# Kernel tuning notes

Hardware: AMD Instinct MI355X
Metric: run time of the kernel (lower is better)

Reference implementation:

```python
import jax, jax.numpy as jnp
import numpy as np

B, T, J, D = 32, 1024, 64, 256


def setup_inputs() -> dict:
    key = jax.random.key(0)
    k1, k2, k3, k4 = jax.random.split(key, 4)
    U = jax.random.normal(k1, (B, J, D), dtype=jnp.float32)
    H = jax.random.normal(k2, (B, T, D), dtype=jnp.float32)
    # similarity_layer: Linear(3*D, 1) -> weight [3*D], bias scalar
    w = jax.random.normal(k3, (3 * D,), dtype=jnp.float32) * (1.0 / np.sqrt(3 * D))
    b = jax.random.normal(k4, (), dtype=jnp.float32) * 0.01
    return {"U": U, "H": H, "w": w, "b": b}


def reference(U, H, w, b):
    # Linear([H; U; H*U]) decomposes exactly into three small contractions:
    # S[b,t,j] = H[b,t]@w_h + U[b,j]@w_u + (H[b,t]*w_hu)@U[b,j] + bias
    w_h, w_u, w_hu = w[:D], w[D:2 * D], w[2 * D:]
    S = (
        jnp.einsum("btd,d->bt", H, w_h)[:, :, None]
        + jnp.einsum("bjd,d->bj", U, w_u)[:, None, :]
        + jnp.einsum("btd,bjd->btj", H * w_hu, U)
        + b
    )  # [B, T, J]
    A = jax.nn.softmax(S, axis=2)                      # context-to-query attention
    c2q = jnp.einsum("btj,bjd->btd", A, U)             # [B, T, D]
    b_att = jax.nn.softmax(jnp.max(S, axis=2), axis=1)  # [B, T]
    q2c = jnp.einsum("bt,btd->bd", b_att, H)[:, None, :]  # [B, 1, D]
    G = jnp.concatenate((H, c2q, H * c2q, H * q2c), axis=2)  # [B, T, 4D]
    return (G, c2q, q2c)
```

## Files before the change

### kernel.cpp

```cpp
#include <hip/hip_runtime.h>
#include <hip/hip_bf16.h>

#define BB 32
#define TT 1024
#define JJ 64
#define DD 256

typedef __attribute__((ext_vector_type(4))) float f32x4;
__device__ __forceinline__ void nt_store4(float* addr, float4 v) {
    union { float4 a; f32x4 b; } u;
    u.a = v;
    __builtin_nontemporal_store(u.b, (f32x4*)addr);
}

__global__ __launch_bounds__(256) void k0_prep(const float* __restrict__ U,
                                               const float* __restrict__ H,
                                               const float* __restrict__ w,
                                               const float* __restrict__ bp,
                                               float* __restrict__ Up,
                                               float* __restrict__ uw,
                                               float* __restrict__ hw) {
    const int wave = threadIdx.x >> 6;
    const int lane = threadIdx.x & 63;
    if (blockIdx.x < 512) {
        const int row = blockIdx.x * 4 + wave;
        float4 u   = *(const float4*)(U + (size_t)row * DD + lane * 4);
        float4 whu = *(const float4*)(w + 2 * DD + lane * 4);
        float4 wu  = *(const float4*)(w + DD + lane * 4);
        float4 o;
        o.x = u.x * whu.x; o.y = u.y * whu.y; o.z = u.z * whu.z; o.w = u.w * whu.w;
        *(float4*)(Up + (size_t)row * DD + lane * 4) = o;
        float p = fmaf(u.x, wu.x, fmaf(u.y, wu.y, fmaf(u.z, wu.z, u.w * wu.w)));
        #pragma unroll
        for (int m = 32; m >= 1; m >>= 1) p += __shfl_xor(p, m, 64);
        if (lane == 0) uw[row] = p + bp[0];
    } else {
        const int base = (blockIdx.x - 512) * 64 + wave * 16;
        float4 wh = *(const float4*)(w + lane * 4);
        float pr[16];
        #pragma unroll
        for (int r = 0; r < 16; ++r) {
            float4 h = *(const float4*)(H + (size_t)(base + r) * DD + lane * 4);
            pr[r] = fmaf(h.x, wh.x, fmaf(h.y, wh.y, fmaf(h.z, wh.z, h.w * wh.w)));
        }
        #pragma unroll
        for (int m = 32; m >= 1; m >>= 1) {
            #pragma unroll
            for (int r = 0; r < 16; ++r) pr[r] += __shfl_xor(pr[r], m, 64);
        }
        if (lane == 0) {
            #pragma unroll
            for (int r = 0; r < 16; ++r) hw[base + r] = pr[r];
        }
    }
}

__global__ __launch_bounds__(512, 6) void k1_main(const float* __restrict__ H,
                                                  const float* __restrict__ U,
                                                  const float* __restrict__ Up,
                                                  const float* __restrict__ uw,
                                                  const float* __restrict__ hw,
                                                  float* __restrict__ m_ws,
                                                  float* __restrict__ G,
                                                  float* __restrict__ c2q_out) {
    __shared__ float lds[10240];
    float* Abuf = lds + 8192;
    const int tid  = threadIdx.x;
    const int lane = tid & 63;
    const int wave = __builtin_amdgcn_readfirstlane(tid >> 6);
    const int b    = blockIdx.x >> 5;
    const int t0   = (blockIdx.x & 31) << 5;
    const int r0   = t0 + wave * 4;
    const float* Hb = H  + (size_t)b * TT * DD;
    const float* Ub = Up + (size_t)b * JJ * DD;
    const float* Ug = U  + (size_t)b * JJ * DD;
    const float uwj = uw[b * JJ + lane];

    float4 pf[4];
    float s0 = 0.f, s1 = 0.f, s2 = 0.f, s3 = 0.f;

    #define PF_LOAD(SRC, HBYTE)                                                          \
        { _Pragma("unroll") for (int i = 0; i < 4; ++i) {                                \
            int idx = i * 512 + tid; int row = idx >> 5, q = idx & 31;                   \
            pf[i] = *(const float4*)((const char*)(SRC) + row * 1024 + (HBYTE) + q * 16); } }
    #define PF_STORE()                                                                   \
        { _Pragma("unroll") for (int i = 0; i < 4; ++i) {                                \
            int idx = i * 512 + tid; int row = idx >> 5, q = idx & 31;                   \
            *(float4*)((char*)lds + row * 512 + ((q * 16) ^ ((row & 7) << 4))) = pf[i]; } }

    #pragma unroll
    for (int i = 0; i < 4; ++i) {
        int idx = i * 512 + tid; int row = idx >> 5, q = idx & 31;
        float4 v = *(const float4*)((const char*)Ub + row * 1024 + q * 16);
        *(float4*)((char*)lds + row * 512 + ((q * 16) ^ ((row & 7) << 4))) = v;
    }
    __syncthreads();

    #define S_HALF(HOFF_F)                                                               \
        { const float* hp0 = Hb + (size_t)(r0 + 0) * DD + (HOFF_F);                      \
          const float* hp1 = Hb + (size_t)(r0 + 1) * DD + (HOFF_F);                      \
          const float* hp2 = Hb + (size_t)(r0 + 2) * DD + (HOFF_F);                      \
          const float* hp3 = Hb + (size_t)(r0 + 3) * DD + (HOFF_F);                      \
          asm volatile("" : "+v"(hp0), "+v"(hp1), "+v"(hp2), "+v"(hp3));                 \
          const char* ur = (const char*)lds + lane * 512;                                \
          const int swz = (lane & 7) << 4;                                               \
          _Pragma("unroll 2") for (int dc = 0; dc < 32; ++dc) {                          \
              float4 u  = *(const float4*)(ur + ((dc * 16) ^ swz));                      \
              float4 x0 = *(const float4*)(hp0 + dc * 4);                                \
              float4 x1 = *(const float4*)(hp1 + dc * 4);                                \
              float4 x2 = *(const float4*)(hp2 + dc * 4);                                \
              float4 x3 = *(const float4*)(hp3 + dc * 4);                                \
              s0 = fmaf(x0.x, u.x, fmaf(x0.y, u.y, fmaf(x0.z, u.z, fmaf(x0.w, u.w, s0))));\
              s1 = fmaf(x1.x, u.x, fmaf(x1.y, u.y, fmaf(x1.z, u.z, fmaf(x1.w, u.w, s1))));\
              s2 = fmaf(x2.x, u.x, fmaf(x2.y, u.y, fmaf(x2.z, u.z, fmaf(x2.w, u.w, s2))));\
              s3 = fmaf(x3.x, u.x, fmaf(x3.y, u.y, fmaf(x3.z, u.z, fmaf(x3.w, u.w, s3))));\
          } }

    PF_LOAD(Ub, 512);
    S_HALF(0);
    __syncthreads();
    PF_STORE();
    __syncthreads();

    PF_LOAD(Ug, 0);
    S_HALF(128);
    {
        float sv0 = s0 + uwj, sv1 = s1 + uwj, sv2 = s2 + uwj, sv3 = s3 + uwj;
        float m0 = sv0, m1 = sv1, m2 = sv2, m3 = sv3;
        #pragma unroll
        for (int m = 32; m >= 1; m >>= 1) {
            m0 = fmaxf(m0, __shfl_xor(m0, m, 64));
            m1 = fmaxf(m1, __shfl_xor(m1, m, 64));
            m2 = fmaxf(m2, __shfl_xor(m2, m, 64));
            m3 = fmaxf(m3, __shfl_xor(m3, m, 64));
        }
        float p0 = __expf(sv0 - m0), p1 = __expf(sv1 - m1);
        float p2 = __expf(sv2 - m2), p3 = __expf(sv3 - m3);
        float l0 = p0, l1 = p1, l2 = p2, l3 = p3;
        #pragma unroll
        for (int m = 32; m >= 1; m >>= 1) {
            l0 += __shfl_xor(l0, m, 64);
            l1 += __shfl_xor(l1, m, 64);
            l2 += __shfl_xor(l2, m, 64);
            l3 += __shfl_xor(l3, m, 64);
        }
        Abuf[(wave * 4 + 0) * 64 + lane] = p0 * (1.0f / l0);
        Abuf[(wave * 4 + 1) * 64 + lane] = p1 * (1.0f / l1);
        Abuf[(wave * 4 + 2) * 64 + lane] = p2 * (1.0f / l2);
        Abuf[(wave * 4 + 3) * 64 + lane] = p3 * (1.0f / l3);
        if (lane == 0) {
            float4 mm;
            mm.x = m0 + hw[b * TT + r0 + 0];
            mm.y = m1 + hw[b * TT + r0 + 1];
            mm.z = m2 + hw[b * TT + r0 + 2];
            mm.w = m3 + hw[b * TT + r0 + 3];
            *(float4*)(m_ws + b * TT + r0) = mm;
        }
    }
    __syncthreads();
    PF_STORE();
    __syncthreads();

    const size_t Gbase = (size_t)b * TT * 1024;

    #define C2Q_HALF(HOFF_F)                                                             \
        { const int q = lane & 31, rh = lane >> 5;                                       \
          float4 a0 = {0.f,0.f,0.f,0.f}, a1 = {0.f,0.f,0.f,0.f};                         \
          const float* Ar0 = Abuf + (wave * 4 + rh) * 64;                                \
          const float* Ar1 = Ar0 + 128;                                                  \
          _Pragma("unroll 2") for (int j = 0; j < 64; ++j) {                             \
              float4 u = *(const float4*)((const char*)lds + j * 512 +                   \
                                          ((q * 16) ^ ((j & 7) << 4)));                  \
              float w0 = Ar0[j], w1 = Ar1[j];                                            \
              a0.x = fmaf(w0, u.x, a0.x); a0.y = fmaf(w0, u.y, a0.y);                    \
              a0.z = fmaf(w0, u.z, a0.z); a0.w = fmaf(w0, u.w, a0.w);                    \
              a1.x = fmaf(w1, u.x, a1.x); a1.y = fmaf(w1, u.y, a1.y);                    \
              a1.z = fmaf(w1, u.z, a1.z); a1.w = fmaf(w1, u.w, a1.w);                    \
          }                                                                              \
          _Pragma("unroll") for (int k = 0; k < 2; ++k) {                                \
              const int row = r0 + rh + 2 * k;                                           \
              float4 c = k ? a1 : a0;                                                    \
              float4 h4 = *(const float4*)(Hb + (size_t)row * DD + (HOFF_F) + q * 4);    \
              float4 hc; hc.x = h4.x * c.x; hc.y = h4.y * c.y;                           \
              hc.z = h4.z * c.z; hc.w = h4.w * c.w;                                      \
              float* Grow = G + Gbase + (size_t)row * 1024 + (HOFF_F) + q * 4;           \
              nt_store4(Grow,       h4);                                                 \
              nt_store4(Grow + 256, c);                                                  \
              nt_store4(Grow + 512, hc);                                                 \
              nt_store4(c2q_out + ((size_t)b * TT + row) * DD + (HOFF_F) + q * 4, c);    \
          } }

    PF_LOAD(Ug, 512);
    C2Q_HALF(0);
    __syncthreads();
    PF_STORE();
    __syncthreads();
    C2Q_HALF(128);

    #undef PF_LOAD
    #undef PF_STORE
    #undef S_HALF
    #undef C2Q_HALF
}

__global__ __launch_bounds__(256) void k2_batt(const float* __restrict__ m_ws,
                                               float* __restrict__ wt,
                                               float* __restrict__ q2c_out) {
    __shared__ float red[256];
    const int b = blockIdx.x, tid = threadIdx.x;
    float v0 = m_ws[b * TT + tid];
    float v1 = m_ws[b * TT + 256 + tid];
    float v2 = m_ws[b * TT + 512 + tid];
    float v3 = m_ws[b * TT + 768 + tid];
    red[tid] = fmaxf(fmaxf(v0, v1), fmaxf(v2, v3));
    __syncthreads();
    for (int s = 128; s >= 1; s >>= 1) {
        if (tid < s) red[tid] = fmaxf(red[tid], red[tid + s]);
        __syncthreads();
    }
    const float M = red[0];
    __syncthreads();
    float e0 = __expf(v0 - M), e1 = __expf(v1 - M), e2 = __expf(v2 - M), e3 = __expf(v3 - M);
    red[tid] = e0 + e1 + e2 + e3;
    __syncthreads();
    for (int s = 128; s >= 1; s >>= 1) {
        if (tid < s) red[tid] += red[tid + s];
        __syncthreads();
    }
    const float iz = 1.0f / red[0];
    wt[b * TT + tid]       = e0 * iz;
    wt[b * TT + 256 + tid] = e1 * iz;
    wt[b * TT + 512 + tid] = e2 * iz;
    wt[b * TT + 768 + tid] = e3 * iz;
    q2c_out[b * DD + tid] = 0.0f;
}

__global__ __launch_bounds__(256) void k2b_q2c(const float* __restrict__ H,
                                               const float* __restrict__ wt,
                                               float* __restrict__ q2c_out) {
    const int b = blockIdx.x >> 5, c = blockIdx.x & 31, tid = threadIdx.x;
    const float* Hb = H + ((size_t)b * TT + c * 32) * DD;
    const float* wb = wt + b * TT + c * 32;
    asm volatile("" : "+v"(wb));
    float acc = 0.f;
    #pragma unroll 8
    for (int i = 0; i < 32; ++i) acc = fmaf(wb[i], Hb[(size_t)i * DD + tid], acc);
    atomicAdd(&q2c_out[b * DD + tid], acc);
}

__global__ __launch_bounds__(256) void k3_gtail(const float* __restrict__ H,
                                                const float* __restrict__ q2c,
                                                float* __restrict__ G) {
    const size_t idx = (size_t)blockIdx.x * 256 + threadIdx.x;
    const int d4 = (int)(idx & 63);
    const size_t bt = idx >> 6;
    const int b = (int)(bt >> 10);
    float4 h = *(const float4*)(H + idx * 4);
    float4 q = *(const float4*)(q2c + (size_t)b * DD + d4 * 4);
    float4 o;
    o.x = h.x * q.x; o.y = h.y * q.y; o.z = h.z * q.z; o.w = h.w * q.w;
    nt_store4(G + bt * 1024 + 768 + d4 * 4, o);
}

extern "C" void kernel_launch(void* const* d_in, const int* in_sizes, int n_in,
                              void* d_out, int out_size, void* d_ws, size_t ws_size,
                              hipStream_t stream) {
    const float* U  = (const float*)d_in[0];
    const float* H  = (const float*)d_in[1];
    const float* w  = (const float*)d_in[2];
    const float* bp = (const float*)d_in[3];
    float* out = (float*)d_out;

    float* G       = out;
    float* c2q_out = out + (size_t)BB * TT * 4 * DD;
    float* q2c_out = c2q_out + (size_t)BB * TT * DD;

    float* Up   = (float*)d_ws;
    float* uwp  = Up + (size_t)BB * JJ * DD;
    float* m_ws = uwp + BB * JJ;
    float* wtp  = m_ws + BB * TT;
    float* hwp  = wtp + BB * TT;

    k0_prep<<<1024, 256, 0, stream>>>(U, H, w, bp, Up, uwp, hwp);
    k1_main<<<BB * (TT / 32), 512, 0, stream>>>(H, U, Up, uwp, hwp, m_ws, G, c2q_out);
    k2_batt<<<BB, 256, 0, stream>>>(m_ws, wtp, q2c_out);
    k2b_q2c<<<BB * 32, 256, 0, stream>>>(H, wtp, q2c_out);
    k3_gtail<<<BB * TT * DD / 4 / 256, 256, 0, stream>>>(H, q2c_out, G);
}
```

Before: 300.9 us.

## Stage H tile in LDS, fold w_hu scaling into S loop, drop Up buffer

After: 264.3 us. -12.2%, faster.

```diff
diff --git a/kernel.cpp b/kernel.cpp
--- a/kernel.cpp
+++ b/kernel.cpp
@@ -6,30 +6,18 @@
 #define JJ 64
 #define DD 256
 
-typedef __attribute__((ext_vector_type(4))) float f32x4;
-__device__ __forceinline__ void nt_store4(float* addr, float4 v) {
-    union { float4 a; f32x4 b; } u;
-    u.a = v;
-    __builtin_nontemporal_store(u.b, (f32x4*)addr);
-}
-
 __global__ __launch_bounds__(256) void k0_prep(const float* __restrict__ U,
                                                const float* __restrict__ H,
                                                const float* __restrict__ w,
                                                const float* __restrict__ bp,
-                                               float* __restrict__ Up,
                                                float* __restrict__ uw,
                                                float* __restrict__ hw) {
     const int wave = threadIdx.x >> 6;
     const int lane = threadIdx.x & 63;
     if (blockIdx.x < 512) {
         const int row = blockIdx.x * 4 + wave;
-        float4 u   = *(const float4*)(U + (size_t)row * DD + lane * 4);
-        float4 whu = *(const float4*)(w + 2 * DD + lane * 4);
-        float4 wu  = *(const float4*)(w + DD + lane * 4);
-        float4 o;
-        o.x = u.x * whu.x; o.y = u.y * whu.y; o.z = u.z * whu.z; o.w = u.w * whu.w;
-        *(float4*)(Up + (size_t)row * DD + lane * 4) = o;
+        float4 u  = *(const float4*)(U + (size_t)row * DD + lane * 4);
+        float4 wu = *(const float4*)(w + DD + lane * 4);
         float p = fmaf(u.x, wu.x, fmaf(u.y, wu.y, fmaf(u.z, wu.z, u.w * wu.w)));
         #pragma unroll
         for (int m = 32; m >= 1; m >>= 1) p += __shfl_xor(p, m, 64);
@@ -55,34 +43,35 @@
     }
 }
 
-__global__ __launch_bounds__(512, 6) void k1_main(const float* __restrict__ H,
+__global__ __launch_bounds__(512, 4) void k1_main(const float* __restrict__ H,
                                                   const float* __restrict__ U,
-                                                  const float* __restrict__ Up,
                                                   const float* __restrict__ uw,
                                                   const float* __restrict__ hw,
+                                                  const float* __restrict__ w,
                                                   float* __restrict__ m_ws,
                                                   float* __restrict__ G,
                                                   float* __restrict__ c2q_out) {
-    __shared__ float lds[10240];
-    float* Abuf = lds + 8192;
+    __shared__ float lds[18688];
+    float* Hs   = lds + 8192;
+    float* Abuf = lds + 16384;
+    float* whuS = lds + 18432;
     const int tid  = threadIdx.x;
     const int lane = tid & 63;
     const int wave = __builtin_amdgcn_readfirstlane(tid >> 6);
     const int b    = blockIdx.x >> 5;
     const int t0   = (blockIdx.x & 31) << 5;
     const int r0   = t0 + wave * 4;
-    const float* Hb = H  + (size_t)b * TT * DD;
-    const float* Ub = Up + (size_t)b * JJ * DD;
-    const float* Ug = U  + (size_t)b * JJ * DD;
+    const float* Hb = H + (size_t)b * TT * DD;
+    const float* Ug = U + (size_t)b * JJ * DD;
     const float uwj = uw[b * JJ + lane];
 
     float4 pf[4];
     float s0 = 0.f, s1 = 0.f, s2 = 0.f, s3 = 0.f;
 
-    #define PF_LOAD(SRC, HBYTE)                                                          \
+    #define PF_LOAD(HBYTE)                                                               \
         { _Pragma("unroll") for (int i = 0; i < 4; ++i) {                                \
             int idx = i * 512 + tid; int row = idx >> 5, q = idx & 31;                   \
-            pf[i] = *(const float4*)((const char*)(SRC) + row * 1024 + (HBYTE) + q * 16); } }
+            pf[i] = *(const float4*)((const char*)Ug + row * 1024 + (HBYTE) + q * 16); } }
     #define PF_STORE()                                                                   \
         { _Pragma("unroll") for (int i = 0; i < 4; ++i) {                                \
             int idx = i * 512 + tid; int row = idx >> 5, q = idx & 31;                   \
@@ -91,39 +80,45 @@
     #pragma unroll
     for (int i = 0; i < 4; ++i) {
         int idx = i * 512 + tid; int row = idx >> 5, q = idx & 31;
-        float4 v = *(const float4*)((const char*)Ub + row * 1024 + q * 16);
+        float4 v = *(const float4*)((const char*)Ug + row * 1024 + q * 16);
         *(float4*)((char*)lds + row * 512 + ((q * 16) ^ ((row & 7) << 4))) = v;
     }
-    __syncthreads();
-
-    #define S_HALF(HOFF_F)                                                               \
-        { const float* hp0 = Hb + (size_t)(r0 + 0) * DD + (HOFF_F);                      \
-          const float* hp1 = Hb + (size_t)(r0 + 1) * DD + (HOFF_F);                      \
-          const float* hp2 = Hb + (size_t)(r0 + 2) * DD + (HOFF_F);                      \
-          const float* hp3 = Hb + (size_t)(r0 + 3) * DD + (HOFF_F);                      \
-          asm volatile("" : "+v"(hp0), "+v"(hp1), "+v"(hp2), "+v"(hp3));                 \
-          const char* ur = (const char*)lds + lane * 512;                                \
-          const int swz = (lane & 7) << 4;                                               \
+    #pragma unroll
+    for (int i = 0; i < 4; ++i) {
+        int idx = i * 512 + tid; int row = idx >> 6, c = idx & 63;
+        float4 v = *(const float4*)(Hb + (size_t)(t0 + row) * DD + c * 4);
+        *(float4*)(Hs + row * 256 + c * 4) = v;
+    }
+    if (tid < 64) *(float4*)(whuS + tid * 4) = *(const float4*)(w + 2 * DD + tid * 4);
+    __syncthreads();
+
+    #define S_HALF(HOFF_B)                                                               \
+        { const char* ur  = (const char*)lds + lane * 512;                               \
+          const int   swz = (lane & 7) << 4;                                             \
+          const char* hs  = (const char*)Hs + wave * 4096 + (HOFF_B);                    \
+          const char* wvp = (const char*)whuS + (HOFF_B);                                \
           _Pragma("unroll 2") for (int dc = 0; dc < 32; ++dc) {                          \
-              float4 u  = *(const float4*)(ur + ((dc * 16) ^ swz));                      \
-              float4 x0 = *(const float4*)(hp0 + dc * 4);                                \
-              float4 x1 = *(const float4*)(hp1 + dc * 4);                                \
-              float4 x2 = *(const float4*)(hp2 + dc * 4);                                \
-              float4 x3 = *(const float4*)(hp3 + dc * 4);                                \
+              float4 ua = *(const float4*)(ur + ((dc * 16) ^ swz));                      \
+              float4 wv = *(const float4*)(wvp + dc * 16);                               \
+              float4 u; u.x = ua.x * wv.x; u.y = ua.y * wv.y;                            \
+              u.z = ua.z * wv.z; u.w = ua.w * wv.w;                                      \
+              float4 x0 = *(const float4*)(hs + dc * 16);                                \
+              float4 x1 = *(const float4*)(hs + 1024 + dc * 16);                         \
+              float4 x2 = *(const float4*)(hs + 2048 + dc * 16);                         \
+              float4 x3 = *(const float4*)(hs + 3072 + dc * 16);                         \
               s0 = fmaf(x0.x, u.x, fmaf(x0.y, u.y, fmaf(x0.z, u.z, fmaf(x0.w, u.w, s0))));\
               s1 = fmaf(x1.x, u.x, fmaf(x1.y, u.y, fmaf(x1.z, u.z, fmaf(x1.w, u.w, s1))));\
               s2 = fmaf(x2.x, u.x, fmaf(x2.y, u.y, fmaf(x2.z, u.z, fmaf(x2.w, u.w, s2))));\
               s3 = fmaf(x3.x, u.x, fmaf(x3.y, u.y, fmaf(x3.z, u.z, fmaf(x3.w, u.w, s3))));\
           } }
 
-    PF_LOAD(Ub, 512);
+    PF_LOAD(512);
     S_HALF(0);
     __syncthreads();
     PF_STORE();
     __syncthreads();
 
-    PF_LOAD(Ug, 0);
-    S_HALF(128);
+    S_HALF(512);
     {
         float sv0 = s0 + uwj, sv1 = s1 + uwj, sv2 = s2 + uwj, sv3 = s3 + uwj;
         float m0 = sv0, m1 = sv1, m2 = sv2, m3 = sv3;
@@ -158,12 +153,10 @@
         }
     }
     __syncthreads();
-    PF_STORE();
-    __syncthreads();
 
     const size_t Gbase = (size_t)b * TT * 1024;
 
-    #define C2Q_HALF(HOFF_F)                                                             \
+    #define C2Q_HALF(HOFF_B, HOFF_F)                                                     \
         { const int q = lane & 31, rh = lane >> 5;                                       \
           float4 a0 = {0.f,0.f,0.f,0.f}, a1 = {0.f,0.f,0.f,0.f};                         \
           const float* Ar0 = Abuf + (wave * 4 + rh) * 64;                                \
@@ -178,24 +171,26 @@
               a1.z = fmaf(w1, u.z, a1.z); a1.w = fmaf(w1, u.w, a1.w);                    \
           }                                                                              \
           _Pragma("unroll") for (int k = 0; k < 2; ++k) {                                \
-              const int row = r0 + rh + 2 * k;                                           \
+              const int lr  = wave * 4 + rh + 2 * k;                                     \
+              const int row = t0 + lr;                                                   \
               float4 c = k ? a1 : a0;                                                    \
-              float4 h4 = *(const float4*)(Hb + (size_t)row * DD + (HOFF_F) + q * 4);    \
+              float4 h4 = *(const float4*)((const char*)Hs + lr * 1024 +                 \
+                                           (HOFF_B) + q * 16);                           \
               float4 hc; hc.x = h4.x * c.x; hc.y = h4.y * c.y;                           \
               hc.z = h4.z * c.z; hc.w = h4.w * c.w;                                      \
               float* Grow = G + Gbase + (size_t)row * 1024 + (HOFF_F) + q * 4;           \
-              nt_store4(Grow,       h4);                                                 \
-              nt_store4(Grow + 256, c);                                                  \
-              nt_store4(Grow + 512, hc);                                                 \
-              nt_store4(c2q_out + ((size_t)b * TT + row) * DD + (HOFF_F) + q * 4, c);    \
+              *(float4*)(Grow)       = h4;                                               \
+              *(float4*)(Grow + 256) = c;                                                \
+              *(float4*)(Grow + 512) = hc;                                               \
+              *(float4*)(c2q_out + ((size_t)b * TT + row) * DD + (HOFF_F) + q * 4) = c;  \
           } }
 
-    PF_LOAD(Ug, 512);
-    C2Q_HALF(0);
+    PF_LOAD(0);
+    C2Q_HALF(512, 128);
     __syncthreads();
     PF_STORE();
     __syncthreads();
-    C2Q_HALF(128);
+    C2Q_HALF(0, 0);
 
     #undef PF_LOAD
     #undef PF_STORE
@@ -259,7 +254,7 @@
     float4 q = *(const float4*)(q2c + (size_t)b * DD + d4 * 4);
     float4 o;
     o.x = h.x * q.x; o.y = h.y * q.y; o.z = h.z * q.z; o.w = h.w * q.w;
-    nt_store4(G + bt * 1024 + 768 + d4 * 4, o);
+    *(float4*)(G + bt * 1024 + 768 + d4 * 4) = o;
 }
 
 extern "C" void kernel_launch(void* const* d_in, const int* in_sizes, int n_in,
@@ -275,14 +270,13 @@
     float* c2q_out = out + (size_t)BB * TT * 4 * DD;
     float* q2c_out = c2q_out + (size_t)BB * TT * DD;
 
-    float* Up   = (float*)d_ws;
-    float* uwp  = Up + (size_t)BB * JJ * DD;
+    float* uwp  = (float*)d_ws;
     float* m_ws = uwp + BB * JJ;
     float* wtp  = m_ws + BB * TT;
     float* hwp  = wtp + BB * TT;
 
-    k0_prep<<<1024, 256, 0, stream>>>(U, H, w, bp, Up, uwp, hwp);
-    k1_main<<<BB * (TT / 32), 512, 0, stream>>>(H, U, Up, uwp, hwp, m_ws, G, c2q_out);
+    k0_prep<<<1024, 256, 0, stream>>>(U, H, w, bp, uwp, hwp);
+    k1_main<<<BB * (TT / 32), 512, 0, stream>>>(H, U, uwp, hwp, w, m_ws, G, c2q_out);
     k2_batt<<<BB, 256, 0, stream>>>(m_ws, wtp, q2c_out);
     k2b_q2c<<<BB * 32, 256, 0, stream>>>(H, wtp, q2c_out);
     k3_gtail<<<BB * TT * DD / 4 / 256, 256, 0, stream>>>(H, q2c_out, G);
```
